# Optimization experiments

Measured on AMD Instinct MI355X. Metric: run time of the kernel, lower is better.

Reference implementation:

```python
import jax, jax.numpy as jnp
import numpy as np

N, E, D = 50000, 300000, 256
BN_EPS = 1e-5


def setup_inputs() -> dict:
    key = jax.random.key(0)
    ks = jax.random.split(key, 8)
    s = 1.0 / np.sqrt(D)
    return {
        'x': jax.random.normal(ks[0], (N, D), dtype=jnp.float32),
        'edge_index': jax.random.randint(ks[1], (2, E), 0, N, dtype=jnp.int64),
        'edge_attr': jax.random.normal(ks[2], (E, D), dtype=jnp.float32),
        'W1': jax.random.normal(ks[3], (D, D), dtype=jnp.float32) * s,
        'b1': jnp.zeros((D,), jnp.float32),
        'W2': jax.random.normal(ks[4], (D, D), dtype=jnp.float32) * s,
        'b2': jnp.zeros((D,), jnp.float32),
        'bn1_gamma': jnp.ones((D,), jnp.float32),
        'bn1_beta': jnp.zeros((D,), jnp.float32),
        'bn1_mean': jnp.zeros((D,), jnp.float32),
        'bn1_var': jnp.ones((D,), jnp.float32),
        'bn2_gamma': jnp.ones((D,), jnp.float32),
        'bn2_beta': jnp.zeros((D,), jnp.float32),
        'bn2_mean': jnp.zeros((D,), jnp.float32),
        'bn2_var': jnp.ones((D,), jnp.float32),
    }


def _bn(z, gamma, beta, mean, var):
    # eval-mode BatchNorm1d
    return (z - mean) * jax.lax.rsqrt(var + BN_EPS) * gamma + beta


def reference(x, edge_index, edge_attr, W1, b1, W2, b2,
              bn1_gamma, bn1_beta, bn1_mean, bn1_var,
              bn2_gamma, bn2_beta, bn2_mean, bn2_var):
    src, dst = edge_index[0], edge_index[1]
    # GINEConv message: relu(x_j + edge_attr), scatter-sum at destination
    msg = jax.nn.relu(x[src] + edge_attr)                      # [E, D]
    agg = jax.ops.segment_sum(msg, dst, num_segments=x.shape[0])  # [N, D]
    conv_out = x + agg            # (1+eps)*x + agg, eps=0; nn=Dropout is identity in eval
    h = x + conv_out              # residual: data.x + conv output
    # FFN: BN -> Linear -> GELU -> Linear
    f = _bn(h, bn1_gamma, bn1_beta, bn1_mean, bn1_var)
    f = jax.nn.gelu(f @ W1.T + b1, approximate=False)
    f = f @ W2.T + b2
    return _bn(h + f, bn2_gamma, bn2_beta, bn2_mean, bn2_var)
```

## Files before the change

### kernel.cpp

```cpp
#include <hip/hip_runtime.h>
#include <hip/hip_bf16.h>
#include <math.h>

#define D 256
#define D4 64

typedef __attribute__((ext_vector_type(8))) short bf16x8;
typedef __attribute__((ext_vector_type(4))) float f32x4;

__device__ inline unsigned short f2bf(float f) {
    union { float f; unsigned u; } v; v.f = f;
    unsigned r = v.u + 0x7fffu + ((v.u >> 16) & 1u);
    return (unsigned short)(r >> 16);
}

__global__ __launch_bounds__(256) void k_prep(
    const float* __restrict__ W1, const float* __restrict__ W2,
    unsigned short* __restrict__ W1b, unsigned short* __restrict__ W2b,
    const float* g1, const float* be1, const float* m1, const float* v1,
    const float* g2, const float* be2, const float* m2, const float* v2,
    float* s1, float* sh1, float* s2, float* sh2)
{
    int i = blockIdx.x * 256 + threadIdx.x;
    if (i < D * D) {
        W1b[i] = f2bf(W1[i]);
        W2b[i] = f2bf(W2[i]);
    }
    if (i < D) {
        float sc1 = g1[i] * rsqrtf(v1[i] + 1e-5f);
        s1[i] = sc1; sh1[i] = be1[i] - m1[i] * sc1;
        float sc2 = g2[i] * rsqrtf(v2[i] + 1e-5f);
        s2[i] = sc2; sh2[i] = be2[i] - m2[i] * sc2;
    }
}

__global__ __launch_bounds__(256) void k_zero(int* counts, int* cursor, int n) {
    int i = blockIdx.x * 256 + threadIdx.x;
    if (i < n) { counts[i] = 0; cursor[i] = 0; }
}

__global__ __launch_bounds__(256) void k_hist(const int* __restrict__ ei, int* counts, int E_) {
    int e = blockIdx.x * 256 + threadIdx.x;
    if (e < E_) atomicAdd(&counts[ei[E_ + e]], 1);
}

__global__ __launch_bounds__(256) void k_scan1(const int* __restrict__ counts,
                                               int* offs, int* partials, int n) {
    __shared__ int tmp[256];
    int tid = threadIdx.x, i = blockIdx.x * 256 + tid;
    int v = (i < n) ? counts[i] : 0;
    tmp[tid] = v; __syncthreads();
    for (int d = 1; d < 256; d <<= 1) {
        int t = (tid >= d) ? tmp[tid - d] : 0;
        __syncthreads();
        tmp[tid] += t;
        __syncthreads();
    }
    if (i < n) offs[i] = tmp[tid] - v;
    if (tid == 255) partials[blockIdx.x] = tmp[255];
}

__global__ __launch_bounds__(256) void k_scan2(int* partials, int nb) {
    __shared__ int tmp[256];
    int tid = threadIdx.x;
    int v = (tid < nb) ? partials[tid] : 0;
    tmp[tid] = v; __syncthreads();
    for (int d = 1; d < 256; d <<= 1) {
        int t = (tid >= d) ? tmp[tid - d] : 0;
        __syncthreads();
        tmp[tid] += t;
        __syncthreads();
    }
    if (tid < nb) partials[tid] = tmp[tid] - v;
}

__global__ __launch_bounds__(256) void k_scan3(int* offs, const int* __restrict__ partials,
                                               int n, int E_) {
    int i = blockIdx.x * 256 + threadIdx.x;
    if (i < n) offs[i] += partials[blockIdx.x];
    if (i == 0) offs[n] = E_;
}

__global__ __launch_bounds__(256) void k_bucket(const int* __restrict__ ei,
                                                const int* __restrict__ offs,
                                                int* cursor, int* sorted, int E_) {
    int e = blockIdx.x * 256 + threadIdx.x;
    if (e < E_) {
        int d = ei[E_ + e];
        int pos = offs[d] + atomicAdd(&cursor[d], 1);
        sorted[pos] = e;
    }
}

__global__ __launch_bounds__(256) void k_agg(
    const float4* __restrict__ x, const float4* __restrict__ ea,
    const int* __restrict__ ei, const int* __restrict__ offs,
    const int* __restrict__ sorted,
    const float* __restrict__ s1, const float* __restrict__ sh1,
    float4* __restrict__ h, ushort4* __restrict__ abf, int N_, int E_)
{
    int wave = threadIdx.x >> 6, lane = threadIdx.x & 63;
    int row = blockIdx.x * 4 + wave;
    if (row >= N_) return;
    float4 xv = x[(long)row * D4 + lane];
    float ax = 2.f * xv.x, ay = 2.f * xv.y, az = 2.f * xv.z, aw = 2.f * xv.w;
    int b = offs[row], en = offs[row + 1];
    for (int i = b; i < en; ++i) {
        int e = sorted[i];
        int s = ei[e];
        float4 sv = x[(long)s * D4 + lane];
        float4 av = ea[(long)e * D4 + lane];
        ax += fmaxf(sv.x + av.x, 0.f);
        ay += fmaxf(sv.y + av.y, 0.f);
        az += fmaxf(sv.z + av.z, 0.f);
        aw += fmaxf(sv.w + av.w, 0.f);
    }
    h[(long)row * D4 + lane] = make_float4(ax, ay, az, aw);
    float4 sc = ((const float4*)s1)[lane];
    float4 sh = ((const float4*)sh1)[lane];
    ushort4 o;
    o.x = f2bf(ax * sc.x + sh.x);
    o.y = f2bf(ay * sc.y + sh.y);
    o.z = f2bf(az * sc.z + sh.z);
    o.w = f2bf(aw * sc.w + sh.w);
    abf[(long)row * D4 + lane] = o;
}

__device__ inline float gelu_tanh(float t) {
    float z = 0.7978845608028654f * (t + 0.044715f * t * t * t);
    float e = __expf(2.f * z);
    return 0.5f * t * (2.f - 2.f / (e + 1.f));
}

__global__ __launch_bounds__(256) void k_gemm1(
    const unsigned short* __restrict__ A, const unsigned short* __restrict__ W,
    const float* __restrict__ bias, unsigned short* __restrict__ G, int M)
{
    int wave = threadIdx.x >> 6;
    int lane = threadIdx.x & 63;
    int gw = blockIdx.x * 4 + wave;
    int m_base = gw * 16;
    if (m_base >= M) return;
    int l16 = lane & 15, quad = lane >> 4;

    const bf16x8* Arow = (const bf16x8*)(A + ((long)(m_base + l16) * D + quad * 8));
    bf16x8 afrag[8];
#pragma unroll
    for (int s = 0; s < 8; ++s) afrag[s] = Arow[s * 4];

#pragma unroll 2
    for (int nt = 0; nt < 16; ++nt) {
        int ncol = nt * 16 + l16;
        const bf16x8* Wrow = (const bf16x8*)(W + ((long)ncol * D + quad * 8));
        f32x4 acc[4];
#pragma unroll
        for (int c = 0; c < 4; ++c) acc[c] = (f32x4){0.f, 0.f, 0.f, 0.f};
#pragma unroll
        for (int c = 0; c < 4; ++c)
            acc[c] = __builtin_amdgcn_mfma_f32_16x16x32_bf16(afrag[c], Wrow[c * 4], acc[c], 0, 0, 0);
#pragma unroll
        for (int c = 0; c < 4; ++c)
            acc[c] = __builtin_amdgcn_mfma_f32_16x16x32_bf16(afrag[c + 4], Wrow[(c + 4) * 4], acc[c], 0, 0, 0);
        float b = bias[ncol];
#pragma unroll
        for (int r = 0; r < 4; ++r) {
            int row = m_base + quad * 4 + r;
            float t = acc[0][r] + acc[1][r] + acc[2][r] + acc[3][r] + b;
            G[(long)row * D + ncol] = f2bf(gelu_tanh(t));
        }
    }
}

__global__ __launch_bounds__(256) void k_gemm2(
    const unsigned short* __restrict__ A, const unsigned short* __restrict__ W,
    const float* __restrict__ bias, const float* __restrict__ h,
    const float* __restrict__ s2, const float* __restrict__ sh2,
    float* __restrict__ out, int M)
{
    int wave = threadIdx.x >> 6;
    int lane = threadIdx.x & 63;
    int gw = blockIdx.x * 4 + wave;
    int m_base = gw * 16;
    if (m_base >= M) return;
    int l16 = lane & 15, quad = lane >> 4;

    const bf16x8* Arow = (const bf16x8*)(A + ((long)(m_base + l16) * D + quad * 8));
    bf16x8 afrag[8];
#pragma unroll
    for (int s = 0; s < 8; ++s) afrag[s] = Arow[s * 4];

#pragma unroll 2
    for (int nt = 0; nt < 16; ++nt) {
        int ncol = nt * 16 + l16;
        const bf16x8* Wrow = (const bf16x8*)(W + ((long)ncol * D + quad * 8));
        f32x4 acc[4];
#pragma unroll
        for (int c = 0; c < 4; ++c) acc[c] = (f32x4){0.f, 0.f, 0.f, 0.f};
#pragma unroll
        for (int c = 0; c < 4; ++c)
            acc[c] = __builtin_amdgcn_mfma_f32_16x16x32_bf16(afrag[c], Wrow[c * 4], acc[c], 0, 0, 0);
#pragma unroll
        for (int c = 0; c < 4; ++c)
            acc[c] = __builtin_amdgcn_mfma_f32_16x16x32_bf16(afrag[c + 4], Wrow[(c + 4) * 4], acc[c], 0, 0, 0);
        float b = bias[ncol];
        float sc = s2[ncol], sh = sh2[ncol];
#pragma unroll
        for (int r = 0; r < 4; ++r) {
            int row = m_base + quad * 4 + r;
            float f = acc[0][r] + acc[1][r] + acc[2][r] + acc[3][r] + b;
            float t = h[(long)row * D + ncol] + f;
            out[(long)row * D + ncol] = t * sc + sh;
        }
    }
}

extern "C" void kernel_launch(void* const* d_in, const int* in_sizes, int n_in,
                              void* d_out, int out_size, void* d_ws, size_t ws_size,
                              hipStream_t stream) {
    const float* x   = (const float*)d_in[0];
    const int*   ei  = (const int*)d_in[1];
    const float* ea  = (const float*)d_in[2];
    const float* W1  = (const float*)d_in[3];
    const float* b1  = (const float*)d_in[4];
    const float* W2  = (const float*)d_in[5];
    const float* b2  = (const float*)d_in[6];
    const float* g1  = (const float*)d_in[7];
    const float* be1 = (const float*)d_in[8];
    const float* m1  = (const float*)d_in[9];
    const float* v1  = (const float*)d_in[10];
    const float* g2  = (const float*)d_in[11];
    const float* be2 = (const float*)d_in[12];
    const float* m2  = (const float*)d_in[13];
    const float* v2  = (const float*)d_in[14];
    float* out = (float*)d_out;

    int N_ = in_sizes[0] / D;
    int E_ = in_sizes[2] / D;

    char* ws = (char*)d_ws;
    size_t off = 0;
    float* h = (float*)(ws + off);                      off += (size_t)N_ * D * 4;
    unsigned short* abf = (unsigned short*)(ws + off);  off += (size_t)N_ * D * 2;
    unsigned short* gbf = (unsigned short*)(ws + off);  off += (size_t)N_ * D * 2;
    unsigned short* W1b = (unsigned short*)(ws + off);  off += (size_t)D * D * 2;
    unsigned short* W2b = (unsigned short*)(ws + off);  off += (size_t)D * D * 2;
    float* s1  = (float*)(ws + off); off += D * 4;
    float* sh1 = (float*)(ws + off); off += D * 4;
    float* s2  = (float*)(ws + off); off += D * 4;
    float* sh2 = (float*)(ws + off); off += D * 4;

    int* counts   = (int*)gbf;
    int* cursor   = counts + N_;
    int* offs     = cursor + N_;
    int* partials = offs + N_ + 1;
    int* sorted   = partials + 256;

    int nblkN = (N_ + 255) / 256;
    int nblkE = (E_ + 255) / 256;

    k_prep<<<(D * D + 255) / 256, 256, 0, stream>>>(W1, W2, W1b, W2b,
        g1, be1, m1, v1, g2, be2, m2, v2, s1, sh1, s2, sh2);
    k_zero<<<nblkN, 256, 0, stream>>>(counts, cursor, N_);
    k_hist<<<nblkE, 256, 0, stream>>>(ei, counts, E_);
    k_scan1<<<nblkN, 256, 0, stream>>>(counts, offs, partials, N_);
    k_scan2<<<1, 256, 0, stream>>>(partials, nblkN);
    k_scan3<<<nblkN, 256, 0, stream>>>(offs, partials, N_, E_);
    k_bucket<<<nblkE, 256, 0, stream>>>(ei, offs, cursor, sorted, E_);
    k_agg<<<(N_ + 3) / 4, 256, 0, stream>>>((const float4*)x, (const float4*)ea,
        ei, offs, sorted, s1, sh1, (float4*)h, (ushort4*)abf, N_, E_);

    int nwaves = (N_ + 15) / 16;
    int gblocks = (nwaves + 3) / 4;
    k_gemm1<<<gblocks, 256, 0, stream>>>(abf, W1b, b1, gbf, N_);
    k_gemm2<<<gblocks, 256, 0, stream>>>(gbf, W2b, b2, h, s2, sh2, out, N_);
}
```

Baseline: 695.5 us.

## Fuse both FFN GEMMs through LDS and rebuild residual from bf16 activations

```diff
diff --git a/kernel.cpp b/kernel.cpp
--- a/kernel.cpp
+++ b/kernel.cpp
@@ -4,6 +4,7 @@
 
 #define D 256
 #define D4 64
+#define GSTRIDE 264
 
 typedef __attribute__((ext_vector_type(8))) short bf16x8;
 typedef __attribute__((ext_vector_type(4))) float f32x4;
@@ -12,6 +13,14 @@
     union { float f; unsigned u; } v; v.f = f;
     unsigned r = v.u + 0x7fffu + ((v.u >> 16) & 1u);
     return (unsigned short)(r >> 16);
+}
+__device__ inline float bf2f(unsigned short u) {
+    union { unsigned u; float f; } v; v.u = ((unsigned)u) << 16; return v.f;
+}
+__device__ inline float gelu_tanh(float t) {
+    float z = 0.7978845608028654f * (t + 0.044715f * t * t * t);
+    float e = __expf(2.f * z);
+    return 0.5f * t * (2.f - 2.f / (e + 1.f));
 }
 
 __global__ __launch_bounds__(256) void k_prep(
@@ -19,24 +28,21 @@
     unsigned short* __restrict__ W1b, unsigned short* __restrict__ W2b,
     const float* g1, const float* be1, const float* m1, const float* v1,
     const float* g2, const float* be2, const float* m2, const float* v2,
-    float* s1, float* sh1, float* s2, float* sh2)
+    float* s1, float* sh1, float* r1, float* s2, float* sh2,
+    int* counts, int* cursor, int N_)
 {
     int i = blockIdx.x * 256 + threadIdx.x;
     if (i < D * D) {
         W1b[i] = f2bf(W1[i]);
         W2b[i] = f2bf(W2[i]);
     }
+    if (i < N_) { counts[i] = 0; cursor[i] = 0; }
     if (i < D) {
         float sc1 = g1[i] * rsqrtf(v1[i] + 1e-5f);
-        s1[i] = sc1; sh1[i] = be1[i] - m1[i] * sc1;
+        s1[i] = sc1; sh1[i] = be1[i] - m1[i] * sc1; r1[i] = 1.f / sc1;
         float sc2 = g2[i] * rsqrtf(v2[i] + 1e-5f);
         s2[i] = sc2; sh2[i] = be2[i] - m2[i] * sc2;
     }
-}
-
-__global__ __launch_bounds__(256) void k_zero(int* counts, int* cursor, int n) {
-    int i = blockIdx.x * 256 + threadIdx.x;
-    if (i < n) { counts[i] = 0; cursor[i] = 0; }
 }
 
 __global__ __launch_bounds__(256) void k_hist(const int* __restrict__ ei, int* counts, int E_) {
@@ -83,21 +89,20 @@
 
 __global__ __launch_bounds__(256) void k_bucket(const int* __restrict__ ei,
                                                 const int* __restrict__ offs,
-                                                int* cursor, int* sorted, int E_) {
+                                                int* cursor, int2* sorted, int E_) {
     int e = blockIdx.x * 256 + threadIdx.x;
     if (e < E_) {
         int d = ei[E_ + e];
         int pos = offs[d] + atomicAdd(&cursor[d], 1);
-        sorted[pos] = e;
+        sorted[pos] = make_int2(ei[e], e);
     }
 }
 
 __global__ __launch_bounds__(256) void k_agg(
     const float4* __restrict__ x, const float4* __restrict__ ea,
-    const int* __restrict__ ei, const int* __restrict__ offs,
-    const int* __restrict__ sorted,
+    const int* __restrict__ offs, const int2* __restrict__ sorted,
     const float* __restrict__ s1, const float* __restrict__ sh1,
-    float4* __restrict__ h, ushort4* __restrict__ abf, int N_, int E_)
+    ushort4* __restrict__ abf, int N_)
 {
     int wave = threadIdx.x >> 6, lane = threadIdx.x & 63;
     int row = blockIdx.x * 4 + wave;
@@ -106,16 +111,14 @@
     float ax = 2.f * xv.x, ay = 2.f * xv.y, az = 2.f * xv.z, aw = 2.f * xv.w;
     int b = offs[row], en = offs[row + 1];
     for (int i = b; i < en; ++i) {
-        int e = sorted[i];
-        int s = ei[e];
-        float4 sv = x[(long)s * D4 + lane];
-        float4 av = ea[(long)e * D4 + lane];
+        int2 se = sorted[i];
+        float4 sv = x[(long)se.x * D4 + lane];
+        float4 av = ea[(long)se.y * D4 + lane];
         ax += fmaxf(sv.x + av.x, 0.f);
         ay += fmaxf(sv.y + av.y, 0.f);
         az += fmaxf(sv.z + av.z, 0.f);
         aw += fmaxf(sv.w + av.w, 0.f);
     }
-    h[(long)row * D4 + lane] = make_float4(ax, ay, az, aw);
     float4 sc = ((const float4*)s1)[lane];
     float4 sh = ((const float4*)sh1)[lane];
     ushort4 o;
@@ -126,90 +129,68 @@
     abf[(long)row * D4 + lane] = o;
 }
 
-__device__ inline float gelu_tanh(float t) {
-    float z = 0.7978845608028654f * (t + 0.044715f * t * t * t);
-    float e = __expf(2.f * z);
-    return 0.5f * t * (2.f - 2.f / (e + 1.f));
-}
-
-__global__ __launch_bounds__(256) void k_gemm1(
-    const unsigned short* __restrict__ A, const unsigned short* __restrict__ W,
-    const float* __restrict__ bias, unsigned short* __restrict__ G, int M)
+__global__ __launch_bounds__(256) void k_ffn(
+    const unsigned short* __restrict__ A,
+    const unsigned short* __restrict__ W1,
+    const unsigned short* __restrict__ W2,
+    const float* __restrict__ b1, const float* __restrict__ b2,
+    const float* __restrict__ r1, const float* __restrict__ sh1,
+    const float* __restrict__ s2, const float* __restrict__ sh2,
+    float* __restrict__ out, int M)
 {
-    int wave = threadIdx.x >> 6;
-    int lane = threadIdx.x & 63;
-    int gw = blockIdx.x * 4 + wave;
-    int m_base = gw * 16;
+    __shared__ __align__(16) unsigned short Gs[4][16][GSTRIDE];
+    int wave = threadIdx.x >> 6, lane = threadIdx.x & 63;
+    int m_base = (blockIdx.x * 4 + wave) * 16;
     if (m_base >= M) return;
     int l16 = lane & 15, quad = lane >> 4;
 
     const bf16x8* Arow = (const bf16x8*)(A + ((long)(m_base + l16) * D + quad * 8));
-    bf16x8 afrag[8];
-#pragma unroll
-    for (int s = 0; s < 8; ++s) afrag[s] = Arow[s * 4];
+    bf16x8 frag[8];
+#pragma unroll
+    for (int s = 0; s < 8; ++s) frag[s] = Arow[s * 4];
 
 #pragma unroll 2
     for (int nt = 0; nt < 16; ++nt) {
         int ncol = nt * 16 + l16;
-        const bf16x8* Wrow = (const bf16x8*)(W + ((long)ncol * D + quad * 8));
-        f32x4 acc[4];
-#pragma unroll
-        for (int c = 0; c < 4; ++c) acc[c] = (f32x4){0.f, 0.f, 0.f, 0.f};
-#pragma unroll
-        for (int c = 0; c < 4; ++c)
-            acc[c] = __builtin_amdgcn_mfma_f32_16x16x32_bf16(afrag[c], Wrow[c * 4], acc[c], 0, 0, 0);
-#pragma unroll
-        for (int c = 0; c < 4; ++c)
-            acc[c] = __builtin_amdgcn_mfma_f32_16x16x32_bf16(afrag[c + 4], Wrow[(c + 4) * 4], acc[c], 0, 0, 0);
-        float b = bias[ncol];
+        const bf16x8* Wrow = (const bf16x8*)(W1 + ((long)ncol * D + quad * 8));
+        f32x4 acc0 = {0.f, 0.f, 0.f, 0.f};
+        f32x4 acc1 = {0.f, 0.f, 0.f, 0.f};
+#pragma unroll
+        for (int s = 0; s < 8; s += 2) {
+            acc0 = __builtin_amdgcn_mfma_f32_16x16x32_bf16(frag[s],     Wrow[s * 4],       acc0, 0, 0, 0);
+            acc1 = __builtin_amdgcn_mfma_f32_16x16x32_bf16(frag[s + 1], Wrow[(s + 1) * 4], acc1, 0, 0, 0);
+        }
+        float b = b1[ncol];
 #pragma unroll
         for (int r = 0; r < 4; ++r) {
-            int row = m_base + quad * 4 + r;
-            float t = acc[0][r] + acc[1][r] + acc[2][r] + acc[3][r] + b;
-            G[(long)row * D + ncol] = f2bf(gelu_tanh(t));
-        }
-    }
-}
-
-__global__ __launch_bounds__(256) void k_gemm2(
-    const unsigned short* __restrict__ A, const unsigned short* __restrict__ W,
-    const float* __restrict__ bias, const float* __restrict__ h,
-    const float* __restrict__ s2, const float* __restrict__ sh2,
-    float* __restrict__ out, int M)
-{
-    int wave = threadIdx.x >> 6;
-    int lane = threadIdx.x & 63;
-    int gw = blockIdx.x * 4 + wave;
-    int m_base = gw * 16;
-    if (m_base >= M) return;
-    int l16 = lane & 15, quad = lane >> 4;
-
-    const bf16x8* Arow = (const bf16x8*)(A + ((long)(m_base + l16) * D + quad * 8));
-    bf16x8 afrag[8];
-#pragma unroll
-    for (int s = 0; s < 8; ++s) afrag[s] = Arow[s * 4];
+            float t = acc0[r] + acc1[r] + b;
+            Gs[wave][quad * 4 + r][ncol] = f2bf(gelu_tanh(t));
+        }
+    }
+
+#pragma unroll
+    for (int s = 0; s < 8; ++s)
+        frag[s] = *(const bf16x8*)&Gs[wave][l16][quad * 8 + s * 32];
 
 #pragma unroll 2
     for (int nt = 0; nt < 16; ++nt) {
         int ncol = nt * 16 + l16;
-        const bf16x8* Wrow = (const bf16x8*)(W + ((long)ncol * D + quad * 8));
-        f32x4 acc[4];
-#pragma unroll
-        for (int c = 0; c < 4; ++c) acc[c] = (f32x4){0.f, 0.f, 0.f, 0.f};
-#pragma unroll
-        for (int c = 0; c < 4; ++c)
-            acc[c] = __builtin_amdgcn_mfma_f32_16x16x32_bf16(afrag[c], Wrow[c * 4], acc[c], 0, 0, 0);
-#pragma unroll
-        for (int c = 0; c < 4; ++c)
-            acc[c] = __builtin_amdgcn_mfma_f32_16x16x32_bf16(afrag[c + 4], Wrow[(c + 4) * 4], acc[c], 0, 0, 0);
-        float b = bias[ncol];
-        float sc = s2[ncol], sh = sh2[ncol];
+        const bf16x8* Wrow = (const bf16x8*)(W2 + ((long)ncol * D + quad * 8));
+        f32x4 acc0 = {0.f, 0.f, 0.f, 0.f};
+        f32x4 acc1 = {0.f, 0.f, 0.f, 0.f};
+#pragma unroll
+        for (int s = 0; s < 8; s += 2) {
+            acc0 = __builtin_amdgcn_mfma_f32_16x16x32_bf16(frag[s],     Wrow[s * 4],       acc0, 0, 0, 0);
+            acc1 = __builtin_amdgcn_mfma_f32_16x16x32_bf16(frag[s + 1], Wrow[(s + 1) * 4], acc1, 0, 0, 0);
+        }
+        float b = b2[ncol], rr = r1[ncol], sh = sh1[ncol];
+        float c2 = s2[ncol], h2 = sh2[ncol];
 #pragma unroll
         for (int r = 0; r < 4; ++r) {
             int row = m_base + quad * 4 + r;
-            float f = acc[0][r] + acc[1][r] + acc[2][r] + acc[3][r] + b;
-            float t = h[(long)row * D + ncol] + f;
-            out[(long)row * D + ncol] = t * sc + sh;
+            float f = acc0[r] + acc1[r] + b;
+            float hv = (bf2f(A[(long)row * D + ncol]) - sh) * rr;
+            out[(long)row * D + ncol] = (hv + f) * c2 + h2;
         }
     }
 }
@@ -239,38 +220,34 @@
 
     char* ws = (char*)d_ws;
     size_t off = 0;
-    float* h = (float*)(ws + off);                      off += (size_t)N_ * D * 4;
     unsigned short* abf = (unsigned short*)(ws + off);  off += (size_t)N_ * D * 2;
-    unsigned short* gbf = (unsigned short*)(ws + off);  off += (size_t)N_ * D * 2;
     unsigned short* W1b = (unsigned short*)(ws + off);  off += (size_t)D * D * 2;
     unsigned short* W2b = (unsigned short*)(ws + off);  off += (size_t)D * D * 2;
     float* s1  = (float*)(ws + off); off += D * 4;
     float* sh1 = (float*)(ws + off); off += D * 4;
+    float* r1  = (float*)(ws + off); off += D * 4;
     float* s2  = (float*)(ws + off); off += D * 4;
     float* sh2 = (float*)(ws + off); off += D * 4;
-
-    int* counts   = (int*)gbf;
-    int* cursor   = counts + N_;
-    int* offs     = cursor + N_;
-    int* partials = offs + N_ + 1;
-    int* sorted   = partials + 256;
+    int* counts   = (int*)(ws + off); off += (size_t)N_ * 4;
+    int* cursor   = (int*)(ws + off); off += (size_t)N_ * 4;
+    int* offs     = (int*)(ws + off); off += (size_t)(N_ + 1) * 4;
+    int* partials = (int*)(ws + off); off += 256 * 4;
+    int2* sorted  = (int2*)(ws + off); off += (size_t)E_ * 8;
 
     int nblkN = (N_ + 255) / 256;
     int nblkE = (E_ + 255) / 256;
 
     k_prep<<<(D * D + 255) / 256, 256, 0, stream>>>(W1, W2, W1b, W2b,
-        g1, be1, m1, v1, g2, be2, m2, v2, s1, sh1, s2, sh2);
-    k_zero<<<nblkN, 256, 0, stream>>>(counts, cursor, N_);
+        g1, be1, m1, v1, g2, be2, m2, v2, s1, sh1, r1, s2, sh2, counts, cursor, N_);
     k_hist<<<nblkE, 256, 0, stream>>>(ei, counts, E_);
     k_scan1<<<nblkN, 256, 0, stream>>>(counts, offs, partials, N_);
     k_scan2<<<1, 256, 0, stream>>>(partials, nblkN);
     k_scan3<<<nblkN, 256, 0, stream>>>(offs, partials, N_, E_);
     k_bucket<<<nblkE, 256, 0, stream>>>(ei, offs, cursor, sorted, E_);
     k_agg<<<(N_ + 3) / 4, 256, 0, stream>>>((const float4*)x, (const float4*)ea,
-        ei, offs, sorted, s1, sh1, (float4*)h, (ushort4*)abf, N_, E_);
-
-    int nwaves = (N_ + 15) / 16;
-    int gblocks = (nwaves + 3) / 4;
-    k_gemm1<<<gblocks, 256, 0, stream>>>(abf, W1b, b1, gbf, N_);
-    k_gemm2<<<gblocks, 256, 0, stream>>>(gbf, W2b, b2, h, s2, sh2, out, N_);
-}
+        offs, sorted, s1, sh1, (ushort4*)abf, N_);
+
+    int mtiles = (N_ + 15) / 16;
+    k_ffn<<<(mtiles + 3) / 4, 256, 0, stream>>>(abf, W1b, W2b, b1, b2,
+        r1, sh1, s2, sh2, out, N_);
+}
```

Measured after the change: 655.4 us. -5.8%, faster.
